# Optimization experiments

Hardware: AMD Instinct MI355X
Metric: run time of the kernel (lower is better)

The kernel has to match this reference:

```python
import jax, jax.numpy as jnp
import numpy as np

N_NODES = 100000
N_EDGES = 1600000
IN_CH = 128
OUT_CH = 64
NEG_SLOPE = 0.2
EPS = 1e-16


def setup_inputs() -> dict:
    key = jax.random.key(0)
    k1, k2, k3, k4 = jax.random.split(key, 4)
    x = jax.random.normal(k1, (N_NODES, IN_CH), dtype=jnp.float32)
    # torch Linear weight layout: [out, in], xavier-ish scale
    W = jax.random.normal(k2, (OUT_CH, IN_CH), dtype=jnp.float32) * (1.0 / np.sqrt(IN_CH))
    att = jax.random.normal(k3, (1, 2 * OUT_CH), dtype=jnp.float32) * 0.1
    edge_index = jax.random.randint(k4, (2, N_EDGES), 0, N_NODES, dtype=jnp.int64)
    return {"x": x, "W": W, "att": att, "edge_index": edge_index}


def reference(x, W, att, edge_index):
    # h = linear(x), no bias
    h = x @ W.T                      # [N, out]
    row, col = edge_index[0], edge_index[1]
    # (cat([h[row], h[col]]) * att).sum(-1) == (h @ att_src)[row] + (h @ att_dst)[col]
    att_src = att[0, :OUT_CH]
    att_dst = att[0, OUT_CH:]
    s_src = h @ att_src              # [N]
    s_dst = h @ att_dst              # [N]
    e = s_src[row] + s_dst[col]      # [E]
    alpha = jnp.exp(jax.nn.leaky_relu(e, negative_slope=NEG_SLOPE))
    denom = jax.ops.segment_sum(alpha, col, num_segments=N_NODES)   # [N]
    alpha = alpha / (denom[col] + EPS)                              # [E]
    msg = alpha[:, None] * h[row]                                   # [E, out]
    out = jax.ops.segment_sum(msg, col, num_segments=N_NODES)      # [N, out]
    return out
```

## Files before the change

### kernel.cpp

```cpp
#include <hip/hip_runtime.h>

#define N_NODES 100000
#define N_EDGES 1600000
#define IN_CH 128
#define OUT_CH 64
#define NEG_SLOPE 0.2f
#define EPS 1e-16f

#define B_SHIFT 10
#define NB 98
#define CAP 17408
#define EPB 2048
#define NBLK_BIN 782

#define PROJ_TILE 64
#define NBLK_PROJ 1563
#define XPAD 132

__global__ __launch_bounds__(256) void k_wt(
    const float* __restrict__ W, float* __restrict__ Wt)
{
    const int tid = blockIdx.x * 256 + threadIdx.x;
    if (tid < OUT_CH * IN_CH) {
        const int c = tid >> 7;
        const int k = tid & (IN_CH - 1);
        Wt[k * OUT_CH + c] = W[tid];
    }
}

__global__ __launch_bounds__(256, 4) void k_proj(
    const float* __restrict__ x, const float* __restrict__ Wt,
    const float* __restrict__ att,
    float* __restrict__ h, float* __restrict__ ssrc, float* __restrict__ sdst)
{
    __shared__ float xs[PROJ_TILE][XPAD];
    __shared__ float ws[IN_CH][OUT_CH];
    const int t = threadIdx.x;
    const int gbase = blockIdx.x * PROJ_TILE;

#pragma unroll
    for (int i = 0; i < 8; ++i) {
        const int f4 = i * 256 + t;
        const int k  = f4 >> 4;
        const int c0 = (f4 & 15) * 4;
        *reinterpret_cast<float4*>(&ws[k][c0]) =
            *reinterpret_cast<const float4*>(Wt + k * OUT_CH + c0);
    }
#pragma unroll
    for (int i = 0; i < 8; ++i) {
        const int f4 = i * 256 + t;
        const int n  = f4 >> 5;
        const int k0 = (f4 & 31) * 4;
        float4 v = make_float4(0.f, 0.f, 0.f, 0.f);
        if (gbase + n < N_NODES)
            v = *reinterpret_cast<const float4*>(
                    x + (size_t)(gbase + n) * IN_CH + k0);
        *reinterpret_cast<float4*>(&xs[n][k0]) = v;
    }
    __syncthreads();

    const int cg = t & 15;
    const int ng = t >> 4;
    const int c0 = cg * 4;

    float acc[4][4];
#pragma unroll
    for (int i = 0; i < 4; ++i)
#pragma unroll
        for (int j = 0; j < 4; ++j) acc[i][j] = 0.f;

#pragma unroll 1
    for (int k4 = 0; k4 < IN_CH / 4; ++k4) {
        float4 xr[4], wr[4];
#pragma unroll
        for (int i = 0; i < 4; ++i)
            xr[i] = *reinterpret_cast<const float4*>(&xs[ng * 4 + i][k4 * 4]);
#pragma unroll
        for (int j = 0; j < 4; ++j)
            wr[j] = *reinterpret_cast<const float4*>(&ws[k4 * 4 + j][c0]);
#pragma unroll
        for (int i = 0; i < 4; ++i) {
#pragma unroll
            for (int j = 0; j < 4; ++j) {
                const float xe = j == 0 ? xr[i].x : j == 1 ? xr[i].y
                               : j == 2 ? xr[i].z : xr[i].w;
                acc[i][0] = fmaf(xe, wr[j].x, acc[i][0]);
                acc[i][1] = fmaf(xe, wr[j].y, acc[i][1]);
                acc[i][2] = fmaf(xe, wr[j].z, acc[i][2]);
                acc[i][3] = fmaf(xe, wr[j].w, acc[i][3]);
            }
        }
    }

    const float as0 = att[c0],          as1 = att[c0 + 1];
    const float as2 = att[c0 + 2],      as3 = att[c0 + 3];
    const float ad0 = att[OUT_CH + c0],     ad1 = att[OUT_CH + c0 + 1];
    const float ad2 = att[OUT_CH + c0 + 2], ad3 = att[OUT_CH + c0 + 3];

#pragma unroll
    for (int i = 0; i < 4; ++i) {
        const int n = gbase + ng * 4 + i;
        if (n < N_NODES) {
            *reinterpret_cast<float4*>(h + (size_t)n * OUT_CH + c0) =
                make_float4(acc[i][0], acc[i][1], acc[i][2], acc[i][3]);
        }
        float ps = acc[i][0] * as0 + acc[i][1] * as1
                 + acc[i][2] * as2 + acc[i][3] * as3;
        float pd = acc[i][0] * ad0 + acc[i][1] * ad1
                 + acc[i][2] * ad2 + acc[i][3] * ad3;
        ps += __shfl_xor(ps, 1); pd += __shfl_xor(pd, 1);
        ps += __shfl_xor(ps, 2); pd += __shfl_xor(pd, 2);
        ps += __shfl_xor(ps, 4); pd += __shfl_xor(pd, 4);
        ps += __shfl_xor(ps, 8); pd += __shfl_xor(pd, 8);
        if (cg == 0 && n < N_NODES) { ssrc[n] = ps; sdst[n] = pd; }
    }
}

__global__ __launch_bounds__(256) void k_bin(
    const int* __restrict__ ei, int* __restrict__ gcnt,
    int* __restrict__ gbuckets)
{
    __shared__ int hist[NB], base[NB], offs[NB];
    const int t = threadIdx.x;
    for (int i = t; i < NB; i += 256) hist[i] = 0;
    __syncthreads();

    const int e0 = blockIdx.x * EPB;
#pragma unroll
    for (int i = 0; i < 2; ++i) {
        const int e = e0 + (i * 256 + t) * 4;
        if (e + 4 <= N_EDGES) {
            const int4 c4 = *reinterpret_cast<const int4*>(ei + N_EDGES + e);
            atomicAdd(hist + (c4.x >> B_SHIFT), 1);
            atomicAdd(hist + (c4.y >> B_SHIFT), 1);
            atomicAdd(hist + (c4.z >> B_SHIFT), 1);
            atomicAdd(hist + (c4.w >> B_SHIFT), 1);
        }
    }
    __syncthreads();

    for (int i = t; i < NB; i += 256) {
        base[i] = atomicAdd(gcnt + i, hist[i]);
        offs[i] = 0;
    }
    __syncthreads();

#pragma unroll
    for (int i = 0; i < 2; ++i) {
        const int e = e0 + (i * 256 + t) * 4;
        if (e + 4 <= N_EDGES) {
            const int4 c4 = *reinterpret_cast<const int4*>(ei + N_EDGES + e);
            const int4 r4 = *reinterpret_cast<const int4*>(ei + e);
            int b, p;
            b = c4.x >> B_SHIFT; p = base[b] + atomicAdd(offs + b, 1);
            if (p < CAP) gbuckets[b * CAP + p] = (r4.x << B_SHIFT) | (c4.x & 1023);
            b = c4.y >> B_SHIFT; p = base[b] + atomicAdd(offs + b, 1);
            if (p < CAP) gbuckets[b * CAP + p] = (r4.y << B_SHIFT) | (c4.y & 1023);
            b = c4.z >> B_SHIFT; p = base[b] + atomicAdd(offs + b, 1);
            if (p < CAP) gbuckets[b * CAP + p] = (r4.z << B_SHIFT) | (c4.z & 1023);
            b = c4.w >> B_SHIFT; p = base[b] + atomicAdd(offs + b, 1);
            if (p < CAP) gbuckets[b * CAP + p] = (r4.w << B_SHIFT) | (c4.w & 1023);
        }
    }
}

__global__ __launch_bounds__(128) void k_scanb(
    const int* __restrict__ gcnt, int* __restrict__ bstart)
{
    __shared__ int lds[128];
    const int t = threadIdx.x;
    const int v = (t < NB) ? gcnt[t] : 0;
    lds[t] = v;
    __syncthreads();
    for (int off = 1; off < 128; off <<= 1) {
        const int add = (t >= off) ? lds[t - off] : 0;
        __syncthreads();
        lds[t] += add;
        __syncthreads();
    }
    if (t < NB) bstart[t] = lds[t] - v;
}

__global__ __launch_bounds__(1024) void k_csr(
    const int* __restrict__ gbuckets, const int* __restrict__ gcnt,
    const int* __restrict__ bstart,
    int* __restrict__ offsets, int* __restrict__ srow)
{
    __shared__ int counts[1024];
    __shared__ int scan[1024];
    const int t = threadIdx.x;
    const int b = blockIdx.x;
    int cnt = gcnt[b]; if (cnt > CAP) cnt = CAP;
    const int bs = bstart[b];
    const int* __restrict__ bucket = gbuckets + (size_t)b * CAP;

    counts[t] = 0;
    __syncthreads();
    for (int j = t; j < cnt; j += 1024)
        atomicAdd(counts + (bucket[j] & 1023), 1);
    __syncthreads();

    const int c = counts[t];
    scan[t] = c;
    __syncthreads();
    for (int off = 1; off < 1024; off <<= 1) {
        const int add = (t >= off) ? scan[t - off] : 0;
        __syncthreads();
        scan[t] += add;
        __syncthreads();
    }
    const int excl = scan[t] - c;
    offsets[b * 1024 + t] = bs + excl;
    counts[t] = excl;
    __syncthreads();

    for (int j = t; j < cnt; j += 1024) {
        const int p = bucket[j];
        const int pos = bs + atomicAdd(counts + (p & 1023), 1);
        srow[pos] = p >> B_SHIFT;
    }
}

__global__ __launch_bounds__(256) void k_gather(
    const int* __restrict__ srow, const int* __restrict__ offsets,
    const float* __restrict__ h,
    const float* __restrict__ ssrc, const float* __restrict__ sdst,
    float* __restrict__ out)
{
    const int lane = threadIdx.x & 63;
    const int c = blockIdx.x * 4 + (threadIdx.x >> 6);
    if (c >= N_NODES) return;

    const int start = __builtin_amdgcn_readfirstlane(offsets[c]);
    const int end   = __builtin_amdgcn_readfirstlane(offsets[c + 1]);
    const float sd = sdst[c];

    float acc0 = 0.f, acc1 = 0.f, acc2 = 0.f, acc3 = 0.f;
    float den0 = 0.f, den1 = 0.f, den2 = 0.f, den3 = 0.f;

    int j = start;
    const int end4 = start + ((end - start) & ~3);
    for (; j < end4; j += 4) {
        const int r0 = __builtin_amdgcn_readfirstlane(srow[j + 0]);
        const int r1 = __builtin_amdgcn_readfirstlane(srow[j + 1]);
        const int r2 = __builtin_amdgcn_readfirstlane(srow[j + 2]);
        const int r3 = __builtin_amdgcn_readfirstlane(srow[j + 3]);

        const float h0 = h[(size_t)r0 * OUT_CH + lane];
        const float h1 = h[(size_t)r1 * OUT_CH + lane];
        const float h2 = h[(size_t)r2 * OUT_CH + lane];
        const float h3 = h[(size_t)r3 * OUT_CH + lane];

        const float s0 = ssrc[r0] + sd;
        const float s1 = ssrc[r1] + sd;
        const float s2 = ssrc[r2] + sd;
        const float s3 = ssrc[r3] + sd;
        const float a0 = __expf(s0 > 0.f ? s0 : s0 * NEG_SLOPE);
        const float a1 = __expf(s1 > 0.f ? s1 : s1 * NEG_SLOPE);
        const float a2 = __expf(s2 > 0.f ? s2 : s2 * NEG_SLOPE);
        const float a3 = __expf(s3 > 0.f ? s3 : s3 * NEG_SLOPE);

        acc0 = fmaf(a0, h0, acc0); den0 += a0;
        acc1 = fmaf(a1, h1, acc1); den1 += a1;
        acc2 = fmaf(a2, h2, acc2); den2 += a2;
        acc3 = fmaf(a3, h3, acc3); den3 += a3;
    }
    for (; j < end; ++j) {
        const int r = __builtin_amdgcn_readfirstlane(srow[j]);
        const float hv = h[(size_t)r * OUT_CH + lane];
        const float s = ssrc[r] + sd;
        const float a = __expf(s > 0.f ? s : s * NEG_SLOPE);
        acc0 = fmaf(a, hv, acc0); den0 += a;
    }

    const float acc = (acc0 + acc1) + (acc2 + acc3);
    const float den = (den0 + den1) + (den2 + den3);
    out[(size_t)c * OUT_CH + lane] = acc / (den + EPS);
}

extern "C" void kernel_launch(void* const* d_in, const int* in_sizes, int n_in,
                              void* d_out, int out_size, void* d_ws, size_t ws_size,
                              hipStream_t stream) {
    const float* x   = (const float*)d_in[0];
    const float* W   = (const float*)d_in[1];
    const float* att = (const float*)d_in[2];
    const int*   ei  = (const int*)d_in[3];
    float* out = (float*)d_out;

    char* ws = (char*)d_ws;
    size_t off = 0;
    auto carve = [&](size_t bytes) {
        void* p = ws + off;
        off += (bytes + 255) & ~(size_t)255;
        return p;
    };
    float* h        = (float*)carve((size_t)N_NODES * OUT_CH * 4);
    float* ssrc     = (float*)carve(N_NODES * 4);
    float* sdst     = (float*)carve(N_NODES * 4);
    float* Wt       = (float*)carve((size_t)IN_CH * OUT_CH * 4);
    int*   gbuckets = (int*)carve((size_t)NB * CAP * 4);
    int*   gcnt     = (int*)carve(NB * 4);
    int*   bstart   = (int*)carve(NB * 4);
    int*   offsets  = (int*)carve((NB * 1024 + 4) * 4);
    int*   srow     = (int*)carve((size_t)N_EDGES * 4);

    hipMemsetAsync(gcnt, 0, NB * sizeof(int), stream);

    k_wt<<<(OUT_CH * IN_CH + 255) / 256, 256, 0, stream>>>(W, Wt);
    k_proj<<<NBLK_PROJ, 256, 0, stream>>>(x, Wt, att, h, ssrc, sdst);
    k_bin<<<NBLK_BIN, 256, 0, stream>>>(ei, gcnt, gbuckets);
    k_scanb<<<1, 128, 0, stream>>>(gcnt, bstart);
    k_csr<<<NB, 1024, 0, stream>>>(gbuckets, gcnt, bstart, offsets, srow);
    k_gather<<<(N_NODES + 3) / 4, 256, 0, stream>>>(srow, offsets,
                                                    h, ssrc, sdst, out);
}
```

Baseline: 242.3 us.

## Precompute edge attention weights in CSR build and vectorize gather loads

The per-edge exp(leaky_relu(ssrc[row]+sdst[col])) is now computed once in the CSR scatter kernel, with sdst cached in LDS, and written to a new alpha array aligned with srow. The gather kernel then reads alpha with float4 and srow with int4 loads, after a peel loop that aligns to 4, instead of doing random ssrc lookups and exps. The block scan in k_csr is replaced by a wavefront shuffle scan plus a 16-entry LDS pass. In exchange, alpha adds an extra 6.4MB write and read, and k_csr gains random ssrc reads and scattered writes while running on only 98 blocks.

```diff
diff --git a/kernel.cpp b/kernel.cpp
--- a/kernel.cpp
+++ b/kernel.cpp
@@ -184,16 +184,23 @@
 __global__ __launch_bounds__(1024) void k_csr(
     const int* __restrict__ gbuckets, const int* __restrict__ gcnt,
     const int* __restrict__ bstart,
-    int* __restrict__ offsets, int* __restrict__ srow)
+    const float* __restrict__ ssrc, const float* __restrict__ sdst,
+    int* __restrict__ offsets, int* __restrict__ srow,
+    float* __restrict__ alpha)
 {
     __shared__ int counts[1024];
-    __shared__ int scan[1024];
+    __shared__ int wsum[16];
+    __shared__ float sdl[1024];
     const int t = threadIdx.x;
+    const int lane = t & 63;
+    const int wid  = t >> 6;
     const int b = blockIdx.x;
     int cnt = gcnt[b]; if (cnt > CAP) cnt = CAP;
     const int bs = bstart[b];
     const int* __restrict__ bucket = gbuckets + (size_t)b * CAP;
 
+    const int node = b * 1024 + t;
+    sdl[t] = (node < N_NODES) ? sdst[node] : 0.f;
     counts[t] = 0;
     __syncthreads();
     for (int j = t; j < cnt; j += 1024)
@@ -201,31 +208,39 @@
     __syncthreads();
 
     const int c = counts[t];
-    scan[t] = c;
-    __syncthreads();
-    for (int off = 1; off < 1024; off <<= 1) {
-        const int add = (t >= off) ? scan[t - off] : 0;
-        __syncthreads();
-        scan[t] += add;
-        __syncthreads();
-    }
-    const int excl = scan[t] - c;
+    int v = c;
+#pragma unroll
+    for (int off = 1; off < 64; off <<= 1) {
+        const int u = __shfl_up(v, off);
+        if (lane >= off) v += u;
+    }
+    if (lane == 63) wsum[wid] = v;
+    __syncthreads();
+    if (t == 0) {
+        int a = 0;
+#pragma unroll
+        for (int i = 0; i < 16; ++i) { const int x = wsum[i]; wsum[i] = a; a += x; }
+    }
+    __syncthreads();
+    const int excl = v + wsum[wid] - c;
     offsets[b * 1024 + t] = bs + excl;
     counts[t] = excl;
     __syncthreads();
 
     for (int j = t; j < cnt; j += 1024) {
         const int p = bucket[j];
+        const int row = p >> B_SHIFT;
         const int pos = bs + atomicAdd(counts + (p & 1023), 1);
-        srow[pos] = p >> B_SHIFT;
+        srow[pos] = row;
+        const float s = ssrc[row] + sdl[p & 1023];
+        alpha[pos] = __expf(s > 0.f ? s : s * NEG_SLOPE);
     }
 }
 
 __global__ __launch_bounds__(256) void k_gather(
-    const int* __restrict__ srow, const int* __restrict__ offsets,
-    const float* __restrict__ h,
-    const float* __restrict__ ssrc, const float* __restrict__ sdst,
-    float* __restrict__ out)
+    const int* __restrict__ srow, const float* __restrict__ alpha,
+    const int* __restrict__ offsets,
+    const float* __restrict__ h, float* __restrict__ out)
 {
     const int lane = threadIdx.x & 63;
     const int c = blockIdx.x * 4 + (threadIdx.x >> 6);
@@ -233,48 +248,46 @@
 
     const int start = __builtin_amdgcn_readfirstlane(offsets[c]);
     const int end   = __builtin_amdgcn_readfirstlane(offsets[c + 1]);
-    const float sd = sdst[c];
 
     float acc0 = 0.f, acc1 = 0.f, acc2 = 0.f, acc3 = 0.f;
-    float den0 = 0.f, den1 = 0.f, den2 = 0.f, den3 = 0.f;
+    float den = 0.f;
 
     int j = start;
-    const int end4 = start + ((end - start) & ~3);
-    for (; j < end4; j += 4) {
-        const int r0 = __builtin_amdgcn_readfirstlane(srow[j + 0]);
-        const int r1 = __builtin_amdgcn_readfirstlane(srow[j + 1]);
-        const int r2 = __builtin_amdgcn_readfirstlane(srow[j + 2]);
-        const int r3 = __builtin_amdgcn_readfirstlane(srow[j + 3]);
+    int peel = (4 - (start & 3)) & 3;
+    if (peel > end - start) peel = end - start;
+    for (int k = 0; k < peel; ++k, ++j) {
+        const int r = __builtin_amdgcn_readfirstlane(srow[j]);
+        const float a = alpha[j];
+        acc0 = fmaf(a, h[(size_t)r * OUT_CH + lane], acc0);
+        den += a;
+    }
+    for (; j + 4 <= end; j += 4) {
+        const int4   r4 = *reinterpret_cast<const int4*>(srow + j);
+        const float4 a4 = *reinterpret_cast<const float4*>(alpha + j);
+        const int r0 = __builtin_amdgcn_readfirstlane(r4.x);
+        const int r1 = __builtin_amdgcn_readfirstlane(r4.y);
+        const int r2 = __builtin_amdgcn_readfirstlane(r4.z);
+        const int r3 = __builtin_amdgcn_readfirstlane(r4.w);
 
         const float h0 = h[(size_t)r0 * OUT_CH + lane];
         const float h1 = h[(size_t)r1 * OUT_CH + lane];
         const float h2 = h[(size_t)r2 * OUT_CH + lane];
         const float h3 = h[(size_t)r3 * OUT_CH + lane];
 
-        const float s0 = ssrc[r0] + sd;
-        const float s1 = ssrc[r1] + sd;
-        const float s2 = ssrc[r2] + sd;
-        const float s3 = ssrc[r3] + sd;
-        const float a0 = __expf(s0 > 0.f ? s0 : s0 * NEG_SLOPE);
-        const float a1 = __expf(s1 > 0.f ? s1 : s1 * NEG_SLOPE);
-        const float a2 = __expf(s2 > 0.f ? s2 : s2 * NEG_SLOPE);
-        const float a3 = __expf(s3 > 0.f ? s3 : s3 * NEG_SLOPE);
-
-        acc0 = fmaf(a0, h0, acc0); den0 += a0;
-        acc1 = fmaf(a1, h1, acc1); den1 += a1;
-        acc2 = fmaf(a2, h2, acc2); den2 += a2;
-        acc3 = fmaf(a3, h3, acc3); den3 += a3;
+        acc0 = fmaf(a4.x, h0, acc0);
+        acc1 = fmaf(a4.y, h1, acc1);
+        acc2 = fmaf(a4.z, h2, acc2);
+        acc3 = fmaf(a4.w, h3, acc3);
+        den += (a4.x + a4.y) + (a4.z + a4.w);
     }
     for (; j < end; ++j) {
         const int r = __builtin_amdgcn_readfirstlane(srow[j]);
-        const float hv = h[(size_t)r * OUT_CH + lane];
-        const float s = ssrc[r] + sd;
-        const float a = __expf(s > 0.f ? s : s * NEG_SLOPE);
-        acc0 = fmaf(a, hv, acc0); den0 += a;
+        const float a = alpha[j];
+        acc0 = fmaf(a, h[(size_t)r * OUT_CH + lane], acc0);
+        den += a;
     }
 
     const float acc = (acc0 + acc1) + (acc2 + acc3);
-    const float den = (den0 + den1) + (den2 + den3);
     out[(size_t)c * OUT_CH + lane] = acc / (den + EPS);
 }
 
@@ -303,6 +316,7 @@
     int*   bstart   = (int*)carve(NB * 4);
     int*   offsets  = (int*)carve((NB * 1024 + 4) * 4);
     int*   srow     = (int*)carve((size_t)N_EDGES * 4);
+    float* alpha    = (float*)carve((size_t)N_EDGES * 4);
 
     hipMemsetAsync(gcnt, 0, NB * sizeof(int), stream);
 
@@ -310,7 +324,8 @@
     k_proj<<<NBLK_PROJ, 256, 0, stream>>>(x, Wt, att, h, ssrc, sdst);
     k_bin<<<NBLK_BIN, 256, 0, stream>>>(ei, gcnt, gbuckets);
     k_scanb<<<1, 128, 0, stream>>>(gcnt, bstart);
-    k_csr<<<NB, 1024, 0, stream>>>(gbuckets, gcnt, bstart, offsets, srow);
-    k_gather<<<(N_NODES + 3) / 4, 256, 0, stream>>>(srow, offsets,
-                                                    h, ssrc, sdst, out);
-}
+    k_csr<<<NB, 1024, 0, stream>>>(gbuckets, gcnt, bstart, ssrc, sdst,
+                                   offsets, srow, alpha);
+    k_gather<<<(N_NODES + 3) / 4, 256, 0, stream>>>(srow, alpha, offsets,
+                                                    h, out);
+}
```

Result: slower. 268.1 us (+10.7%).

## Replace CSR build and gather with bucket-local LDS atomic aggregation

Applied to the files above, without the earlier changes.

Drops the scan, CSR construction and per-node gather kernels. A single kernel now processes each destination bucket of 1024 nodes in two channel halves, accumulating attention-weighted messages and denominators into shared memory with atomics before normalising and writing out. This removes the srow/offsets construction pass and two kernel launches. In exchange it uses only 196 blocks with about 132KB of LDS each, reads each bucket twice, and relies on LDS float atomics, which can be contended and limit parallelism.

```diff
diff --git a/kernel.cpp b/kernel.cpp
--- a/kernel.cpp
+++ b/kernel.cpp
@@ -16,6 +16,8 @@
 #define PROJ_TILE 64
 #define NBLK_PROJ 1563
 #define XPAD 132
+
+#define CHH 32
 
 __global__ __launch_bounds__(256) void k_wt(
     const float* __restrict__ W, float* __restrict__ Wt)
@@ -164,118 +166,69 @@
     }
 }
 
-__global__ __launch_bounds__(128) void k_scanb(
-    const int* __restrict__ gcnt, int* __restrict__ bstart)
-{
-    __shared__ int lds[128];
-    const int t = threadIdx.x;
-    const int v = (t < NB) ? gcnt[t] : 0;
-    lds[t] = v;
-    __syncthreads();
-    for (int off = 1; off < 128; off <<= 1) {
-        const int add = (t >= off) ? lds[t - off] : 0;
-        __syncthreads();
-        lds[t] += add;
-        __syncthreads();
-    }
-    if (t < NB) bstart[t] = lds[t] - v;
-}
-
-__global__ __launch_bounds__(1024) void k_csr(
+__global__ __launch_bounds__(1024, 1) void k_agg(
     const int* __restrict__ gbuckets, const int* __restrict__ gcnt,
-    const int* __restrict__ bstart,
-    int* __restrict__ offsets, int* __restrict__ srow)
-{
-    __shared__ int counts[1024];
-    __shared__ int scan[1024];
-    const int t = threadIdx.x;
-    const int b = blockIdx.x;
-    int cnt = gcnt[b]; if (cnt > CAP) cnt = CAP;
-    const int bs = bstart[b];
-    const int* __restrict__ bucket = gbuckets + (size_t)b * CAP;
-
-    counts[t] = 0;
-    __syncthreads();
-    for (int j = t; j < cnt; j += 1024)
-        atomicAdd(counts + (bucket[j] & 1023), 1);
-    __syncthreads();
-
-    const int c = counts[t];
-    scan[t] = c;
-    __syncthreads();
-    for (int off = 1; off < 1024; off <<= 1) {
-        const int add = (t >= off) ? scan[t - off] : 0;
-        __syncthreads();
-        scan[t] += add;
-        __syncthreads();
-    }
-    const int excl = scan[t] - c;
-    offsets[b * 1024 + t] = bs + excl;
-    counts[t] = excl;
-    __syncthreads();
-
-    for (int j = t; j < cnt; j += 1024) {
-        const int p = bucket[j];
-        const int pos = bs + atomicAdd(counts + (p & 1023), 1);
-        srow[pos] = p >> B_SHIFT;
-    }
-}
-
-__global__ __launch_bounds__(256) void k_gather(
-    const int* __restrict__ srow, const int* __restrict__ offsets,
     const float* __restrict__ h,
     const float* __restrict__ ssrc, const float* __restrict__ sdst,
     float* __restrict__ out)
 {
-    const int lane = threadIdx.x & 63;
-    const int c = blockIdx.x * 4 + (threadIdx.x >> 6);
-    if (c >= N_NODES) return;
-
-    const int start = __builtin_amdgcn_readfirstlane(offsets[c]);
-    const int end   = __builtin_amdgcn_readfirstlane(offsets[c + 1]);
-    const float sd = sdst[c];
-
-    float acc0 = 0.f, acc1 = 0.f, acc2 = 0.f, acc3 = 0.f;
-    float den0 = 0.f, den1 = 0.f, den2 = 0.f, den3 = 0.f;
-
-    int j = start;
-    const int end4 = start + ((end - start) & ~3);
-    for (; j < end4; j += 4) {
-        const int r0 = __builtin_amdgcn_readfirstlane(srow[j + 0]);
-        const int r1 = __builtin_amdgcn_readfirstlane(srow[j + 1]);
-        const int r2 = __builtin_amdgcn_readfirstlane(srow[j + 2]);
-        const int r3 = __builtin_amdgcn_readfirstlane(srow[j + 3]);
-
-        const float h0 = h[(size_t)r0 * OUT_CH + lane];
-        const float h1 = h[(size_t)r1 * OUT_CH + lane];
-        const float h2 = h[(size_t)r2 * OUT_CH + lane];
-        const float h3 = h[(size_t)r3 * OUT_CH + lane];
-
-        const float s0 = ssrc[r0] + sd;
-        const float s1 = ssrc[r1] + sd;
-        const float s2 = ssrc[r2] + sd;
-        const float s3 = ssrc[r3] + sd;
-        const float a0 = __expf(s0 > 0.f ? s0 : s0 * NEG_SLOPE);
-        const float a1 = __expf(s1 > 0.f ? s1 : s1 * NEG_SLOPE);
-        const float a2 = __expf(s2 > 0.f ? s2 : s2 * NEG_SLOPE);
-        const float a3 = __expf(s3 > 0.f ? s3 : s3 * NEG_SLOPE);
-
-        acc0 = fmaf(a0, h0, acc0); den0 += a0;
-        acc1 = fmaf(a1, h1, acc1); den1 += a1;
-        acc2 = fmaf(a2, h2, acc2); den2 += a2;
-        acc3 = fmaf(a3, h3, acc3); den3 += a3;
-    }
-    for (; j < end; ++j) {
-        const int r = __builtin_amdgcn_readfirstlane(srow[j]);
-        const float hv = h[(size_t)r * OUT_CH + lane];
-        const float s = ssrc[r] + sd;
+    __shared__ float acc[1024][CHH];
+    __shared__ float den[1024];
+    __shared__ float sdl[1024];
+    const int t = threadIdx.x;
+    const int b = blockIdx.x >> 1;
+    const int H = blockIdx.x & 1;
+    int cnt = gcnt[b]; if (cnt > CAP) cnt = CAP;
+    const int* __restrict__ bucket = gbuckets + (size_t)b * CAP;
+    const int gnode0 = b << B_SHIFT;
+
+    const int node = gnode0 + t;
+    sdl[t] = (node < N_NODES) ? sdst[node] : 0.f;
+    den[t] = 0.f;
+    float* accf = &acc[0][0];
+    for (int f = t; f < 1024 * CHH; f += 1024) accf[f] = 0.f;
+    __syncthreads();
+
+    const int lane = t & 63;
+    const int wid  = t >> 6;
+    const int half = lane >> 5;
+    const int ch   = lane & 31;
+    const int hoff = H * CHH + ch;
+
+    int j = wid * 2 + half;
+    for (; j + 32 < cnt; j += 64) {
+        const int pA = bucket[j];
+        const int pB = bucket[j + 32];
+        const int rowA = pA >> B_SHIFT, clA = pA & 1023;
+        const int rowB = pB >> B_SHIFT, clB = pB & 1023;
+        const float hA = h[(size_t)rowA * OUT_CH + hoff];
+        const float hB = h[(size_t)rowB * OUT_CH + hoff];
+        const float sA = ssrc[rowA] + sdl[clA];
+        const float sB = ssrc[rowB] + sdl[clB];
+        const float aA = __expf(sA > 0.f ? sA : sA * NEG_SLOPE);
+        const float aB = __expf(sB > 0.f ? sB : sB * NEG_SLOPE);
+        atomicAdd(&acc[clA][ch], aA * hA);
+        atomicAdd(&acc[clB][ch], aB * hB);
+        if (ch == 0) { atomicAdd(&den[clA], aA); atomicAdd(&den[clB], aB); }
+    }
+    for (; j < cnt; j += 32) {
+        const int p = bucket[j];
+        const int row = p >> B_SHIFT, cl = p & 1023;
+        const float hv = h[(size_t)row * OUT_CH + hoff];
+        const float s = ssrc[row] + sdl[cl];
         const float a = __expf(s > 0.f ? s : s * NEG_SLOPE);
-        acc0 = fmaf(a, hv, acc0); den0 += a;
-    }
-
-    const float acc = (acc0 + acc1) + (acc2 + acc3);
-    const float den = (den0 + den1) + (den2 + den3);
-    out[(size_t)c * OUT_CH + lane] = acc / (den + EPS);
+        atomicAdd(&acc[cl][ch], a * hv);
+        if (ch == 0) atomicAdd(&den[cl], a);
+    }
+    __syncthreads();
+
+    for (int f = t; f < 1024 * CHH; f += 1024) {
+        const int n = f >> 5;
+        const int c = f & 31;
+        const int gn = gnode0 + n;
+        if (gn < N_NODES)
+            out[(size_t)gn * OUT_CH + H * CHH + c] = accf[f] / (den[n] + EPS);
+    }
 }
 
 extern "C" void kernel_launch(void* const* d_in, const int* in_sizes, int n_in,
@@ -300,17 +253,11 @@
     float* Wt       = (float*)carve((size_t)IN_CH * OUT_CH * 4);
     int*   gbuckets = (int*)carve((size_t)NB * CAP * 4);
     int*   gcnt     = (int*)carve(NB * 4);
-    int*   bstart   = (int*)carve(NB * 4);
-    int*   offsets  = (int*)carve((NB * 1024 + 4) * 4);
-    int*   srow     = (int*)carve((size_t)N_EDGES * 4);
 
     hipMemsetAsync(gcnt, 0, NB * sizeof(int), stream);
 
     k_wt<<<(OUT_CH * IN_CH + 255) / 256, 256, 0, stream>>>(W, Wt);
     k_proj<<<NBLK_PROJ, 256, 0, stream>>>(x, Wt, att, h, ssrc, sdst);
     k_bin<<<NBLK_BIN, 256, 0, stream>>>(ei, gcnt, gbuckets);
-    k_scanb<<<1, 128, 0, stream>>>(gcnt, bstart);
-    k_csr<<<NB, 1024, 0, stream>>>(gbuckets, gcnt, bstart, offsets, srow);
-    k_gather<<<(N_NODES + 3) / 4, 256, 0, stream>>>(srow, offsets,
-                                                    h, ssrc, sdst, out);
-}
+    k_agg<<<NB * 2, 1024, 0, stream>>>(gbuckets, gcnt, h, ssrc, sdst, out);
+}
```

Result: slower. 882.9 us (+264.4%).

## Use finer 256-node buckets for CSR build with wave-shuffle scan

Applied to the files above, without the earlier changes.

Shrinks the destination bucket width from 1024 to 256 nodes, which gives 392 buckets, so the CSR kernel runs 392 blocks of 256 threads instead of 98 blocks of 1024. The LDS Hillis-Steele scan in that kernel is replaced by a wave-level shuffle scan followed by a small cross-wave combine. Binning blocks now handle 4096 edges each, and the bucket scan is widened to 512 threads. The aim is better GPU occupancy and fewer barriers in CSR construction, at the cost of more global bucket counters and tighter per-bucket capacity margins.

```diff
diff --git a/kernel.cpp b/kernel.cpp
--- a/kernel.cpp
+++ b/kernel.cpp
@@ -7,11 +7,12 @@
 #define NEG_SLOPE 0.2f
 #define EPS 1e-16f
 
-#define B_SHIFT 10
-#define NB 98
-#define CAP 17408
-#define EPB 2048
-#define NBLK_BIN 782
+#define B_SHIFT 8
+#define BMASK 255
+#define NB 392
+#define CAP 4608
+#define EPB 4096
+#define NBLK_BIN 391
 
 #define PROJ_TILE 64
 #define NBLK_PROJ 1563
@@ -127,7 +128,7 @@
 
     const int e0 = blockIdx.x * EPB;
 #pragma unroll
-    for (int i = 0; i < 2; ++i) {
+    for (int i = 0; i < 4; ++i) {
         const int e = e0 + (i * 256 + t) * 4;
         if (e + 4 <= N_EDGES) {
             const int4 c4 = *reinterpret_cast<const int4*>(ei + N_EDGES + e);
@@ -146,33 +147,33 @@
     __syncthreads();
 
 #pragma unroll
-    for (int i = 0; i < 2; ++i) {
+    for (int i = 0; i < 4; ++i) {
         const int e = e0 + (i * 256 + t) * 4;
         if (e + 4 <= N_EDGES) {
             const int4 c4 = *reinterpret_cast<const int4*>(ei + N_EDGES + e);
             const int4 r4 = *reinterpret_cast<const int4*>(ei + e);
             int b, p;
             b = c4.x >> B_SHIFT; p = base[b] + atomicAdd(offs + b, 1);
-            if (p < CAP) gbuckets[b * CAP + p] = (r4.x << B_SHIFT) | (c4.x & 1023);
+            if (p < CAP) gbuckets[b * CAP + p] = (r4.x << B_SHIFT) | (c4.x & BMASK);
             b = c4.y >> B_SHIFT; p = base[b] + atomicAdd(offs + b, 1);
-            if (p < CAP) gbuckets[b * CAP + p] = (r4.y << B_SHIFT) | (c4.y & 1023);
+            if (p < CAP) gbuckets[b * CAP + p] = (r4.y << B_SHIFT) | (c4.y & BMASK);
             b = c4.z >> B_SHIFT; p = base[b] + atomicAdd(offs + b, 1);
-            if (p < CAP) gbuckets[b * CAP + p] = (r4.z << B_SHIFT) | (c4.z & 1023);
+            if (p < CAP) gbuckets[b * CAP + p] = (r4.z << B_SHIFT) | (c4.z & BMASK);
             b = c4.w >> B_SHIFT; p = base[b] + atomicAdd(offs + b, 1);
-            if (p < CAP) gbuckets[b * CAP + p] = (r4.w << B_SHIFT) | (c4.w & 1023);
+            if (p < CAP) gbuckets[b * CAP + p] = (r4.w << B_SHIFT) | (c4.w & BMASK);
         }
     }
 }
 
-__global__ __launch_bounds__(128) void k_scanb(
+__global__ __launch_bounds__(512) void k_scanb(
     const int* __restrict__ gcnt, int* __restrict__ bstart)
 {
-    __shared__ int lds[128];
+    __shared__ int lds[512];
     const int t = threadIdx.x;
     const int v = (t < NB) ? gcnt[t] : 0;
     lds[t] = v;
     __syncthreads();
-    for (int off = 1; off < 128; off <<= 1) {
+    for (int off = 1; off < 512; off <<= 1) {
         const int add = (t >= off) ? lds[t - off] : 0;
         __syncthreads();
         lds[t] += add;
@@ -181,14 +182,16 @@
     if (t < NB) bstart[t] = lds[t] - v;
 }
 
-__global__ __launch_bounds__(1024) void k_csr(
+__global__ __launch_bounds__(256) void k_csr(
     const int* __restrict__ gbuckets, const int* __restrict__ gcnt,
     const int* __restrict__ bstart,
     int* __restrict__ offsets, int* __restrict__ srow)
 {
-    __shared__ int counts[1024];
-    __shared__ int scan[1024];
+    __shared__ int counts[256];
+    __shared__ int wsum[4];
     const int t = threadIdx.x;
+    const int lane = t & 63;
+    const int wid  = t >> 6;
     const int b = blockIdx.x;
     int cnt = gcnt[b]; if (cnt > CAP) cnt = CAP;
     const int bs = bstart[b];
@@ -196,27 +199,33 @@
 
     counts[t] = 0;
     __syncthreads();
-    for (int j = t; j < cnt; j += 1024)
-        atomicAdd(counts + (bucket[j] & 1023), 1);
+    for (int j = t; j < cnt; j += 256)
+        atomicAdd(counts + (bucket[j] & BMASK), 1);
     __syncthreads();
 
     const int c = counts[t];
-    scan[t] = c;
-    __syncthreads();
-    for (int off = 1; off < 1024; off <<= 1) {
-        const int add = (t >= off) ? scan[t - off] : 0;
-        __syncthreads();
-        scan[t] += add;
-        __syncthreads();
-    }
-    const int excl = scan[t] - c;
-    offsets[b * 1024 + t] = bs + excl;
-    counts[t] = excl;
-    __syncthreads();
-
-    for (int j = t; j < cnt; j += 1024) {
+    int v = c;
+#pragma unroll
+    for (int off = 1; off < 64; off <<= 1) {
+        const int u = __shfl_up(v, off);
+        if (lane >= off) v += u;
+    }
+    if (lane == 63) wsum[wid] = v;
+    __syncthreads();
+    if (t == 0) {
+        int a = 0;
+#pragma unroll
+        for (int i = 0; i < 4; ++i) { const int x = wsum[i]; wsum[i] = a; a += x; }
+    }
+    __syncthreads();
+    const int excl = v + wsum[wid] - c;
+    offsets[b * 256 + t] = bs + excl;
+    counts[t] = bs + excl;
+    __syncthreads();
+
+    for (int j = t; j < cnt; j += 256) {
         const int p = bucket[j];
-        const int pos = bs + atomicAdd(counts + (p & 1023), 1);
+        const int pos = atomicAdd(counts + (p & BMASK), 1);
         srow[pos] = p >> B_SHIFT;
     }
 }
@@ -301,7 +310,7 @@
     int*   gbuckets = (int*)carve((size_t)NB * CAP * 4);
     int*   gcnt     = (int*)carve(NB * 4);
     int*   bstart   = (int*)carve(NB * 4);
-    int*   offsets  = (int*)carve((NB * 1024 + 4) * 4);
+    int*   offsets  = (int*)carve((NB * 256 + 4) * 4);
     int*   srow     = (int*)carve((size_t)N_EDGES * 4);
 
     hipMemsetAsync(gcnt, 0, NB * sizeof(int), stream);
@@ -309,8 +318,8 @@
     k_wt<<<(OUT_CH * IN_CH + 255) / 256, 256, 0, stream>>>(W, Wt);
     k_proj<<<NBLK_PROJ, 256, 0, stream>>>(x, Wt, att, h, ssrc, sdst);
     k_bin<<<NBLK_BIN, 256, 0, stream>>>(ei, gcnt, gbuckets);
-    k_scanb<<<1, 128, 0, stream>>>(gcnt, bstart);
-    k_csr<<<NB, 1024, 0, stream>>>(gbuckets, gcnt, bstart, offsets, srow);
+    k_scanb<<<1, 512, 0, stream>>>(gcnt, bstart);
+    k_csr<<<NB, 256, 0, stream>>>(gbuckets, gcnt, bstart, offsets, srow);
     k_gather<<<(N_NODES + 3) / 4, 256, 0, stream>>>(srow, offsets,
                                                     h, ssrc, sdst, out);
 }
```

Result: faster. 230.7 us (-4.8%).
